# Optimization experiments

Hardware: AMD Instinct MI355X
Metric: run time of the kernel (lower is better)

## Reference

```python
import jax, jax.numpy as jnp
import numpy as np

NUM_HEADS = 16


def setup_inputs() -> dict:
    key = jax.random.key(0)
    k1, k2, k3 = jax.random.split(key, 3)
    B, S, D = 4, 2048, 1024
    x = jax.random.normal(k1, (B, S, D), dtype=jnp.float32)
    w_qkv = jax.random.normal(k2, (D, 3 * D), dtype=jnp.float32) * 0.02
    b_qkv = jnp.zeros((3 * D,), dtype=jnp.float32)
    w_proj = jax.random.normal(k3, (D, D), dtype=jnp.float32) * 0.02
    b_proj = jnp.zeros((D,), dtype=jnp.float32)
    return {"x": x, "w_qkv": w_qkv, "b_qkv": b_qkv, "w_proj": w_proj, "b_proj": b_proj}


def reference(x, w_qkv, b_qkv, w_proj, b_proj):
    B, S, D = x.shape
    H = NUM_HEADS
    hd = D // H
    # fused qkv projection: [B,S,3D] -> [B,S,3H,hd]
    qkv = (x @ w_qkv + b_qkv).reshape(B, S, 3 * H, hd)
    q, k, v = jnp.split(qkv, 3, axis=2)  # each [B,S,H,hd]
    scale = (1.0 / jnp.sqrt(hd)).astype(x.dtype)
    scores = jnp.einsum("bqhd,bkhd->bhqk", q, k) * scale  # [B,H,S,S]
    causal = jnp.tril(jnp.ones((S, S), dtype=bool))  # [S,S]
    masked = jnp.where(causal, scores, jnp.finfo(scores.dtype).min)
    # softmax in fp32 reduce dtype, cast back (dropout_rate=0 -> identity)
    attn = jax.nn.softmax(masked.astype(jnp.float32)).astype(masked.dtype)
    out = jnp.einsum("bhqk,bkhd->bqhd", attn, v).reshape(B, S, D)
    return out @ w_proj + b_proj
```

## Files before the change

### kernel.cpp

```cpp
#include <hip/hip_runtime.h>
#include <hip/hip_bf16.h>

typedef __attribute__((ext_vector_type(8))) short short8;
typedef __attribute__((ext_vector_type(4))) float f32x4;

#define B_   4
#define S_   2048
#define D_   1024
#define H_   16
#define HD_  64
#define M_   (B_ * S_)
#define N3_  (3 * D_)

#define GLDS16(g, l)                                                        \
  __builtin_amdgcn_global_load_lds(                                         \
      (const __attribute__((address_space(1))) void*)(g),                   \
      (__attribute__((address_space(3))) void*)(l), 16, 0, 0)

__device__ __forceinline__ unsigned pack_bf2(float a, float b) {
  union { __hip_bfloat16 h; unsigned short s; } ua, ub;
  ua.h = __float2bfloat16(a);
  ub.h = __float2bfloat16(b);
  return (unsigned)ua.s | ((unsigned)ub.s << 16);
}

__global__ __launch_bounds__(256) void cast_f32_bf16(
    const float* __restrict__ in, __hip_bfloat16* __restrict__ out, int n) {
  int i = (blockIdx.x * 256 + threadIdx.x) * 4;
  if (i + 3 < n) {
    float4 v = *(const float4*)(in + i);
    union { ushort4 u4; __hip_bfloat16 h[4]; } p;
    p.h[0] = __float2bfloat16(v.x);
    p.h[1] = __float2bfloat16(v.y);
    p.h[2] = __float2bfloat16(v.z);
    p.h[3] = __float2bfloat16(v.w);
    *(ushort4*)(out + i) = p.u4;
  }
}

__global__ __launch_bounds__(256) void transpose_cast(
    const float* __restrict__ in, __hip_bfloat16* __restrict__ out,
    int rows, int cols) {
  __shared__ float tile[32][33];
  int bx = blockIdx.x * 32;
  int by = blockIdx.y * 32;
  int tx = threadIdx.x, ty = threadIdx.y;
#pragma unroll
  for (int i = 0; i < 4; ++i)
    tile[ty + i * 8][tx] = in[(size_t)(by + ty + i * 8) * cols + bx + tx];
  __syncthreads();
#pragma unroll
  for (int i = 0; i < 4; ++i)
    out[(size_t)(bx + ty + i * 8) * rows + by + tx] =
        __float2bfloat16(tile[tx][ty + i * 8]);
}

__device__ inline void store_out(float* p, float v) { *p = v; }
__device__ inline void store_out(__hip_bfloat16* p, float v) {
  *p = __float2bfloat16(v);
}

template <typename OUT_T, bool WVT>
__global__ __launch_bounds__(256) void gemm_bt_bias(
    const __hip_bfloat16* __restrict__ A, const __hip_bfloat16* __restrict__ Bt,
    const float* __restrict__ bias, OUT_T* __restrict__ C,
    __hip_bfloat16* __restrict__ vt, int M, int N, int K) {
  __shared__ __align__(16) __hip_bfloat16 Alds[128 * 64];
  __shared__ __align__(16) __hip_bfloat16 Blds[128 * 64];
  const int t = threadIdx.x;
  const int wave = t >> 6, lane = t & 63;
  const int quad = lane >> 4, l15 = lane & 15;
  const int wm = (wave >> 1) * 64, wn = (wave & 1) * 64;
  const int m0 = blockIdx.y * 128, n0 = blockIdx.x * 128;

  const int rsub = lane >> 3;
  const int gc16 = (lane & 7) ^ (rsub & 7);
  const __hip_bfloat16* gA[4];
  const __hip_bfloat16* gB[4];
  __hip_bfloat16* lA[4];
  __hip_bfloat16* lB[4];
#pragma unroll
  for (int i = 0; i < 4; ++i) {
    int c = wave * 4 + i;
    int row = c * 8 + rsub;
    gA[i] = A + (size_t)(m0 + row) * K + gc16 * 8;
    gB[i] = Bt + (size_t)(n0 + row) * K + gc16 * 8;
    lA[i] = Alds + c * 512;
    lB[i] = Blds + c * 512;
  }

  f32x4 acc[4][4] = {};

  for (int k0 = 0; k0 < K; k0 += 64) {
#pragma unroll
    for (int i = 0; i < 4; ++i) {
      GLDS16(gA[i] + k0, lA[i]);
      GLDS16(gB[i] + k0, lB[i]);
    }
    __syncthreads();
#pragma unroll
    for (int kk = 0; kk < 2; ++kk) {
      const int fo = ((kk * 4 + quad) ^ (l15 & 7)) * 8;
      short8 a[4], bfr[4];
#pragma unroll
      for (int mt = 0; mt < 4; ++mt)
        a[mt] = *(const short8*)(Alds + (wm + mt * 16 + l15) * 64 + fo);
#pragma unroll
      for (int nt = 0; nt < 4; ++nt)
        bfr[nt] = *(const short8*)(Blds + (wn + nt * 16 + l15) * 64 + fo);
#pragma unroll
      for (int mt = 0; mt < 4; ++mt)
#pragma unroll
        for (int nt = 0; nt < 4; ++nt)
          acc[mt][nt] = __builtin_amdgcn_mfma_f32_16x16x32_bf16(
              a[mt], bfr[nt], acc[mt][nt], 0, 0, 0);
    }
    __syncthreads();
  }

  if (WVT && n0 >= 2048) {
#pragma unroll
    for (int mt = 0; mt < 4; ++mt)
#pragma unroll
      for (int nt = 0; nt < 4; ++nt) {
        int col = n0 + wn + nt * 16 + l15;
        float bv = bias[col];
        int hv = (col - 2048) >> 6, d = (col - 2048) & 63;
        int row0 = m0 + wm + mt * 16 + quad * 4;
        int bidx = row0 >> 11, s = row0 & 2047;
        uint2 w;
        w.x = pack_bf2(acc[mt][nt][0] + bv, acc[mt][nt][1] + bv);
        w.y = pack_bf2(acc[mt][nt][2] + bv, acc[mt][nt][3] + bv);
        *(uint2*)(vt + ((size_t)(bidx * 16 + hv) * 64 + d) * 2048 + s) = w;
      }
  } else {
#pragma unroll
    for (int mt = 0; mt < 4; ++mt)
#pragma unroll
      for (int nt = 0; nt < 4; ++nt) {
        int col = n0 + wn + nt * 16 + l15;
        float bv = bias[col];
#pragma unroll
        for (int r = 0; r < 4; ++r) {
          int row = m0 + wm + mt * 16 + quad * 4 + r;
          store_out(C + (size_t)row * N + col, acc[mt][nt][r] + bv);
        }
      }
  }
}

__global__ __launch_bounds__(128) void attn_causal(
    const __hip_bfloat16* __restrict__ qkv,
    const __hip_bfloat16* __restrict__ vt,
    __hip_bfloat16* __restrict__ ctx) {
  __shared__ __align__(16) __hip_bfloat16 Klds[64][72];
  __shared__ __align__(16) __hip_bfloat16 Vlds[64][72];
  __shared__ __align__(16) __hip_bfloat16 Plds[2][2][16][72];

  const int t = threadIdx.x;
  const int wave = t >> 6, lane = t & 63;
  const int quad = lane >> 4, l15 = lane & 15;
  const int xb = blockIdx.x, h = blockIdx.y, b = blockIdx.z;

  const size_t qbase = (size_t)b * S_ * N3_ + h * HD_;
  const size_t kbase = qbase + D_;
  const size_t vtbase = (size_t)(b * H_ + h) * HD_ * S_;
  const float C2 = 0.18033688f;

  short8 ones;
#pragma unroll
  for (int j = 0; j < 8; ++j) ones[j] = (short)0x3F80;

  for (int sel = 0; sel < 2; ++sel) {
    const int qb = sel ? (31 - xb) : xb;
    short8 qf[2][2];
#pragma unroll
    for (int g = 0; g < 2; ++g) {
      const int qrow = qb * 64 + wave * 32 + g * 16 + l15;
      qf[g][0] =
          *(const short8*)(qkv + qbase + (size_t)qrow * N3_ + quad * 8);
      qf[g][1] =
          *(const short8*)(qkv + qbase + (size_t)qrow * N3_ + 32 + quad * 8);
    }

    f32x4 o[2][4] = {};
    float m_r[2] = {-1e30f, -1e30f}, l_r[2] = {0.f, 0.f};

    for (int kb = 0; kb <= qb; ++kb) {
#pragma unroll
      for (int i = 0; i < 4; ++i) {
        int c = t + 128 * i;
        int row = c >> 3, seg = c & 7;
        *(uint4*)(&Klds[row][seg * 8]) = *(const uint4*)(
            qkv + kbase + (size_t)(kb * 64 + row) * N3_ + seg * 8);
        *(uint4*)(&Vlds[row][seg * 8]) = *(const uint4*)(
            vt + vtbase + (size_t)row * S_ + kb * 64 + seg * 8);
      }
      __syncthreads();

      short8 kf[4][2];
#pragma unroll
      for (int nt = 0; nt < 4; ++nt) {
        kf[nt][0] = *(const short8*)(&Klds[nt * 16 + l15][quad * 8]);
        kf[nt][1] = *(const short8*)(&Klds[nt * 16 + l15][32 + quad * 8]);
      }

      const bool diag = (kb == qb);
#pragma unroll
      for (int g = 0; g < 2; ++g) {
        f32x4 st[4];
#pragma unroll
        for (int nt = 0; nt < 4; ++nt) {
          f32x4 z = {};
          z = __builtin_amdgcn_mfma_f32_16x16x32_bf16(kf[nt][0], qf[g][0], z,
                                                      0, 0, 0);
          z = __builtin_amdgcn_mfma_f32_16x16x32_bf16(kf[nt][1], qf[g][1], z,
                                                      0, 0, 0);
          st[nt] = z;
        }
        if (diag) {
          const int rloc = wave * 32 + g * 16 + l15;
#pragma unroll
          for (int nt = 0; nt < 4; ++nt)
#pragma unroll
            for (int r = 0; r < 4; ++r)
              if (nt * 16 + quad * 4 + r > rloc) st[nt][r] = -1e30f;
        }

        float tm = st[0][0];
#pragma unroll
        for (int nt = 0; nt < 4; ++nt)
#pragma unroll
          for (int r = 0; r < 4; ++r) tm = fmaxf(tm, st[nt][r]);
        tm = fmaxf(tm, __shfl_xor(tm, 16));
        tm = fmaxf(tm, __shfl_xor(tm, 32));
        const float mn = fmaxf(m_r[g], tm * C2);
        const float alpha = __builtin_amdgcn_exp2f(m_r[g] - mn);
        m_r[g] = mn;
        l_r[g] *= alpha;

#pragma unroll
        for (int nt = 0; nt < 4; ++nt) {
          float p0 = __builtin_amdgcn_exp2f(__builtin_fmaf(st[nt][0], C2, -mn));
          float p1 = __builtin_amdgcn_exp2f(__builtin_fmaf(st[nt][1], C2, -mn));
          float p2 = __builtin_amdgcn_exp2f(__builtin_fmaf(st[nt][2], C2, -mn));
          float p3 = __builtin_amdgcn_exp2f(__builtin_fmaf(st[nt][3], C2, -mn));
          uint2 w;
          w.x = pack_bf2(p0, p1);
          w.y = pack_bf2(p2, p3);
          *(uint2*)(&Plds[wave][g][l15][nt * 16 + quad * 4]) = w;
        }

#pragma unroll
        for (int dt = 0; dt < 4; ++dt)
#pragma unroll
          for (int r = 0; r < 4; ++r) o[g][dt][r] *= alpha;
      }

      short8 pB[2][2];
#pragma unroll
      for (int g = 0; g < 2; ++g) {
        pB[g][0] = *(const short8*)(&Plds[wave][g][l15][quad * 8]);
        pB[g][1] = *(const short8*)(&Plds[wave][g][l15][32 + quad * 8]);
        f32x4 ps = {};
        ps = __builtin_amdgcn_mfma_f32_16x16x32_bf16(ones, pB[g][0], ps, 0, 0, 0);
        ps = __builtin_amdgcn_mfma_f32_16x16x32_bf16(ones, pB[g][1], ps, 0, 0, 0);
        l_r[g] += ps[0];
      }

#pragma unroll
      for (int dt = 0; dt < 4; ++dt) {
        short8 v0 = *(const short8*)(&Vlds[dt * 16 + l15][quad * 8]);
        short8 v1 = *(const short8*)(&Vlds[dt * 16 + l15][32 + quad * 8]);
#pragma unroll
        for (int g = 0; g < 2; ++g) {
          o[g][dt] = __builtin_amdgcn_mfma_f32_16x16x32_bf16(v0, pB[g][0],
                                                             o[g][dt], 0, 0, 0);
          o[g][dt] = __builtin_amdgcn_mfma_f32_16x16x32_bf16(v1, pB[g][1],
                                                             o[g][dt], 0, 0, 0);
        }
      }
      __syncthreads();
    }

#pragma unroll
    for (int g = 0; g < 2; ++g) {
      const float rl = __builtin_amdgcn_rcpf(l_r[g]);
      const int qrow = qb * 64 + wave * 32 + g * 16 + l15;
      __hip_bfloat16* crow = ctx + ((size_t)b * S_ + qrow) * D_ + h * HD_;
#pragma unroll
      for (int dt = 0; dt < 4; ++dt) {
        uint2 w;
        w.x = pack_bf2(o[g][dt][0] * rl, o[g][dt][1] * rl);
        w.y = pack_bf2(o[g][dt][2] * rl, o[g][dt][3] * rl);
        *(uint2*)(crow + dt * 16 + quad * 4) = w;
      }
    }
  }
}

extern "C" void kernel_launch(void* const* d_in, const int* in_sizes, int n_in,
                              void* d_out, int out_size, void* d_ws,
                              size_t ws_size, hipStream_t stream) {
  const float* x      = (const float*)d_in[0];
  const float* w_qkv  = (const float*)d_in[1];
  const float* b_qkv  = (const float*)d_in[2];
  const float* w_proj = (const float*)d_in[3];
  const float* b_proj = (const float*)d_in[4];
  float* out = (float*)d_out;

  char* ws = (char*)d_ws;
  __hip_bfloat16* xb     = (__hip_bfloat16*)(ws + 0);
  __hip_bfloat16* wqkvT  = (__hip_bfloat16*)(ws + 16777216);
  __hip_bfloat16* wprojT = (__hip_bfloat16*)(ws + 23068672);
  __hip_bfloat16* qkvb   = (__hip_bfloat16*)(ws + 25165824);
  __hip_bfloat16* ctx    = (__hip_bfloat16*)(ws + 75497472);
  __hip_bfloat16* vt2    = (__hip_bfloat16*)(ws + 91750400);

  cast_f32_bf16<<<8192, 256, 0, stream>>>(x, xb, M_ * D_);
  transpose_cast<<<dim3(N3_ / 32, D_ / 32), dim3(32, 8), 0, stream>>>(
      w_qkv, wqkvT, D_, N3_);
  transpose_cast<<<dim3(D_ / 32, D_ / 32), dim3(32, 8), 0, stream>>>(
      w_proj, wprojT, D_, D_);

  gemm_bt_bias<__hip_bfloat16, true>
      <<<dim3(N3_ / 128, M_ / 128), 256, 0, stream>>>(
          xb, wqkvT, b_qkv, qkvb, vt2, M_, N3_, D_);

  attn_causal<<<dim3(16, H_, B_), 128, 0, stream>>>(qkvb, vt2, ctx);

  gemm_bt_bias<float, false><<<dim3(D_ / 128, M_ / 128), 256, 0, stream>>>(
      ctx, wprojT, b_proj, out, (__hip_bfloat16*)nullptr, M_, D_, D_);
}
```

Before: 281.7 us.

## Prefetch K/V via global_load_lds with swizzled LDS and lazy softmax rescale

Restructures the causal attention kernel so the next K/V tile streams into LDS through direct global-to-LDS loads while the current tile is computed, with fragments read into registers before the barrier. Removes LDS row padding in favour of an XOR swizzle, and launches one block per query tile (heaviest first) instead of pairing tiles. Also skips the online-softmax rescale unless the running max grows by more than a threshold. The goal is to hide global load latency and cut per-iteration overhead, at the cost of more registers and a lazy-rescale threshold that could affect numerical range.

```diff
diff --git a/kernel.cpp b/kernel.cpp
--- a/kernel.cpp
+++ b/kernel.cpp
@@ -149,18 +149,19 @@
   }
 }
 
-__global__ __launch_bounds__(128) void attn_causal(
+__global__ __launch_bounds__(128, 3) void attn_causal(
     const __hip_bfloat16* __restrict__ qkv,
     const __hip_bfloat16* __restrict__ vt,
     __hip_bfloat16* __restrict__ ctx) {
-  __shared__ __align__(16) __hip_bfloat16 Klds[64][72];
-  __shared__ __align__(16) __hip_bfloat16 Vlds[64][72];
-  __shared__ __align__(16) __hip_bfloat16 Plds[2][2][16][72];
+  __shared__ __align__(16) __hip_bfloat16 Klds[64 * 64];
+  __shared__ __align__(16) __hip_bfloat16 Vlds[64 * 64];
+  __shared__ __align__(16) __hip_bfloat16 Plds[2][2][16][64];
 
   const int t = threadIdx.x;
   const int wave = t >> 6, lane = t & 63;
   const int quad = lane >> 4, l15 = lane & 15;
-  const int xb = blockIdx.x, h = blockIdx.y, b = blockIdx.z;
+  const int qb = 31 - (int)blockIdx.x;
+  const int h = blockIdx.y, b = blockIdx.z;
 
   const size_t qbase = (size_t)b * S_ * N3_ + h * HD_;
   const size_t kbase = qbase + D_;
@@ -171,130 +172,154 @@
 #pragma unroll
   for (int j = 0; j < 8; ++j) ones[j] = (short)0x3F80;
 
-  for (int sel = 0; sel < 2; ++sel) {
-    const int qb = sel ? (31 - xb) : xb;
-    short8 qf[2][2];
+  short8 qf[2][2];
+#pragma unroll
+  for (int g = 0; g < 2; ++g) {
+    const int qrow = qb * 64 + wave * 32 + g * 16 + l15;
+    qf[g][0] = *(const short8*)(qkv + qbase + (size_t)qrow * N3_ + quad * 8);
+    qf[g][1] =
+        *(const short8*)(qkv + qbase + (size_t)qrow * N3_ + 32 + quad * 8);
+  }
+
+  const int rsub = lane >> 3;
+  const int swz = ((lane & 7) ^ rsub) * 8;
+  const __hip_bfloat16* gK[4];
+  const __hip_bfloat16* gV[4];
+  __hip_bfloat16* lK[4];
+  __hip_bfloat16* lV[4];
+#pragma unroll
+  for (int i = 0; i < 4; ++i) {
+    const int c = wave * 4 + i;
+    gK[i] = qkv + kbase + (size_t)(c * 8 + rsub) * N3_ + swz;
+    gV[i] = vt + vtbase + (size_t)(c * 8 + rsub) * S_ + swz;
+    lK[i] = Klds + c * 512;
+    lV[i] = Vlds + c * 512;
+  }
+
+  f32x4 o[2][4] = {};
+  float m_r[2] = {-1e30f, -1e30f}, l_r[2] = {0.f, 0.f};
+
+  const int fo0 = (quad ^ (l15 & 7)) * 8;
+  const int fo1 = ((4 + quad) ^ (l15 & 7)) * 8;
+
+#pragma unroll
+  for (int i = 0; i < 4; ++i) {
+    GLDS16(gK[i], lK[i]);
+    GLDS16(gV[i], lV[i]);
+  }
+  __syncthreads();
+
+  for (int kb = 0; kb <= qb; ++kb) {
+    short8 kf[4][2], vf[4][2];
+#pragma unroll
+    for (int nt = 0; nt < 4; ++nt) {
+      const __hip_bfloat16* kr = Klds + (nt * 16 + l15) * 64;
+      const __hip_bfloat16* vr = Vlds + (nt * 16 + l15) * 64;
+      kf[nt][0] = *(const short8*)(kr + fo0);
+      kf[nt][1] = *(const short8*)(kr + fo1);
+      vf[nt][0] = *(const short8*)(vr + fo0);
+      vf[nt][1] = *(const short8*)(vr + fo1);
+    }
+    __syncthreads();
+    if (kb < qb) {
+#pragma unroll
+      for (int i = 0; i < 4; ++i) {
+        gK[i] += 64 * N3_;
+        gV[i] += 64;
+        GLDS16(gK[i], lK[i]);
+        GLDS16(gV[i], lV[i]);
+      }
+    }
+
+    const bool diag = (kb == qb);
+    short8 pB[2][2];
 #pragma unroll
     for (int g = 0; g < 2; ++g) {
-      const int qrow = qb * 64 + wave * 32 + g * 16 + l15;
-      qf[g][0] =
-          *(const short8*)(qkv + qbase + (size_t)qrow * N3_ + quad * 8);
-      qf[g][1] =
-          *(const short8*)(qkv + qbase + (size_t)qrow * N3_ + 32 + quad * 8);
-    }
-
-    f32x4 o[2][4] = {};
-    float m_r[2] = {-1e30f, -1e30f}, l_r[2] = {0.f, 0.f};
-
-    for (int kb = 0; kb <= qb; ++kb) {
-#pragma unroll
-      for (int i = 0; i < 4; ++i) {
-        int c = t + 128 * i;
-        int row = c >> 3, seg = c & 7;
-        *(uint4*)(&Klds[row][seg * 8]) = *(const uint4*)(
-            qkv + kbase + (size_t)(kb * 64 + row) * N3_ + seg * 8);
-        *(uint4*)(&Vlds[row][seg * 8]) = *(const uint4*)(
-            vt + vtbase + (size_t)row * S_ + kb * 64 + seg * 8);
-      }
-      __syncthreads();
-
-      short8 kf[4][2];
+      f32x4 st[4];
 #pragma unroll
       for (int nt = 0; nt < 4; ++nt) {
-        kf[nt][0] = *(const short8*)(&Klds[nt * 16 + l15][quad * 8]);
-        kf[nt][1] = *(const short8*)(&Klds[nt * 16 + l15][32 + quad * 8]);
-      }
-
-      const bool diag = (kb == qb);
+        f32x4 z = {};
+        z = __builtin_amdgcn_mfma_f32_16x16x32_bf16(kf[nt][0], qf[g][0], z,
+                                                    0, 0, 0);
+        z = __builtin_amdgcn_mfma_f32_16x16x32_bf16(kf[nt][1], qf[g][1], z,
+                                                    0, 0, 0);
+        st[nt] = z;
+      }
+      if (diag) {
+        const int rloc = wave * 32 + g * 16 + l15;
+#pragma unroll
+        for (int nt = 0; nt < 4; ++nt)
+#pragma unroll
+          for (int r = 0; r < 4; ++r)
+            if (nt * 16 + quad * 4 + r > rloc) st[nt][r] = -1e30f;
+      }
+
+      float tm = st[0][0];
+#pragma unroll
+      for (int nt = 0; nt < 4; ++nt)
+#pragma unroll
+        for (int r = 0; r < 4; ++r) tm = fmaxf(tm, st[nt][r]);
+      tm = fmaxf(tm, __shfl_xor(tm, 16));
+      tm = fmaxf(tm, __shfl_xor(tm, 32));
+      const float pm = tm * C2;
+
+      if (!__all(pm - m_r[g] <= 8.0f)) {
+        const float mn = fmaxf(m_r[g], pm);
+        const float al = __builtin_amdgcn_exp2f(m_r[g] - mn);
+        m_r[g] = mn;
+        l_r[g] *= al;
+#pragma unroll
+        for (int dt = 0; dt < 4; ++dt)
+#pragma unroll
+          for (int r = 0; r < 4; ++r) o[g][dt][r] *= al;
+      }
+      const float mneg = -m_r[g];
+
+      __hip_bfloat16* prow = &Plds[wave][g][l15][0];
+#pragma unroll
+      for (int nt = 0; nt < 4; ++nt) {
+        float p0 = __builtin_amdgcn_exp2f(__builtin_fmaf(st[nt][0], C2, mneg));
+        float p1 = __builtin_amdgcn_exp2f(__builtin_fmaf(st[nt][1], C2, mneg));
+        float p2 = __builtin_amdgcn_exp2f(__builtin_fmaf(st[nt][2], C2, mneg));
+        float p3 = __builtin_amdgcn_exp2f(__builtin_fmaf(st[nt][3], C2, mneg));
+        uint2 w;
+        w.x = pack_bf2(p0, p1);
+        w.y = pack_bf2(p2, p3);
+        const int u = nt * 2 + (quad >> 1);
+        *(uint2*)(prow + ((u ^ (l15 & 7)) * 8 + (quad & 1) * 4)) = w;
+      }
+      pB[g][0] = *(const short8*)(prow + fo0);
+      pB[g][1] = *(const short8*)(prow + fo1);
+
+      f32x4 ps = {};
+      ps = __builtin_amdgcn_mfma_f32_16x16x32_bf16(ones, pB[g][0], ps, 0, 0, 0);
+      ps = __builtin_amdgcn_mfma_f32_16x16x32_bf16(ones, pB[g][1], ps, 0, 0, 0);
+      l_r[g] += ps[0];
+    }
+
+#pragma unroll
+    for (int dt = 0; dt < 4; ++dt)
 #pragma unroll
       for (int g = 0; g < 2; ++g) {
-        f32x4 st[4];
-#pragma unroll
-        for (int nt = 0; nt < 4; ++nt) {
-          f32x4 z = {};
-          z = __builtin_amdgcn_mfma_f32_16x16x32_bf16(kf[nt][0], qf[g][0], z,
-                                                      0, 0, 0);
-          z = __builtin_amdgcn_mfma_f32_16x16x32_bf16(kf[nt][1], qf[g][1], z,
-                                                      0, 0, 0);
-          st[nt] = z;
-        }
-        if (diag) {
-          const int rloc = wave * 32 + g * 16 + l15;
-#pragma unroll
-          for (int nt = 0; nt < 4; ++nt)
-#pragma unroll
-            for (int r = 0; r < 4; ++r)
-              if (nt * 16 + quad * 4 + r > rloc) st[nt][r] = -1e30f;
-        }
-
-        float tm = st[0][0];
-#pragma unroll
-        for (int nt = 0; nt < 4; ++nt)
-#pragma unroll
-          for (int r = 0; r < 4; ++r) tm = fmaxf(tm, st[nt][r]);
-        tm = fmaxf(tm, __shfl_xor(tm, 16));
-        tm = fmaxf(tm, __shfl_xor(tm, 32));
-        const float mn = fmaxf(m_r[g], tm * C2);
-        const float alpha = __builtin_amdgcn_exp2f(m_r[g] - mn);
-        m_r[g] = mn;
-        l_r[g] *= alpha;
-
-#pragma unroll
-        for (int nt = 0; nt < 4; ++nt) {
-          float p0 = __builtin_amdgcn_exp2f(__builtin_fmaf(st[nt][0], C2, -mn));
-          float p1 = __builtin_amdgcn_exp2f(__builtin_fmaf(st[nt][1], C2, -mn));
-          float p2 = __builtin_amdgcn_exp2f(__builtin_fmaf(st[nt][2], C2, -mn));
-          float p3 = __builtin_amdgcn_exp2f(__builtin_fmaf(st[nt][3], C2, -mn));
-          uint2 w;
-          w.x = pack_bf2(p0, p1);
-          w.y = pack_bf2(p2, p3);
-          *(uint2*)(&Plds[wave][g][l15][nt * 16 + quad * 4]) = w;
-        }
-
-#pragma unroll
-        for (int dt = 0; dt < 4; ++dt)
-#pragma unroll
-          for (int r = 0; r < 4; ++r) o[g][dt][r] *= alpha;
-      }
-
-      short8 pB[2][2];
-#pragma unroll
-      for (int g = 0; g < 2; ++g) {
-        pB[g][0] = *(const short8*)(&Plds[wave][g][l15][quad * 8]);
-        pB[g][1] = *(const short8*)(&Plds[wave][g][l15][32 + quad * 8]);
-        f32x4 ps = {};
-        ps = __builtin_amdgcn_mfma_f32_16x16x32_bf16(ones, pB[g][0], ps, 0, 0, 0);
-        ps = __builtin_amdgcn_mfma_f32_16x16x32_bf16(ones, pB[g][1], ps, 0, 0, 0);
-        l_r[g] += ps[0];
-      }
-
-#pragma unroll
-      for (int dt = 0; dt < 4; ++dt) {
-        short8 v0 = *(const short8*)(&Vlds[dt * 16 + l15][quad * 8]);
-        short8 v1 = *(const short8*)(&Vlds[dt * 16 + l15][32 + quad * 8]);
-#pragma unroll
-        for (int g = 0; g < 2; ++g) {
-          o[g][dt] = __builtin_amdgcn_mfma_f32_16x16x32_bf16(v0, pB[g][0],
-                                                             o[g][dt], 0, 0, 0);
-          o[g][dt] = __builtin_amdgcn_mfma_f32_16x16x32_bf16(v1, pB[g][1],
-                                                             o[g][dt], 0, 0, 0);
-        }
-      }
-      __syncthreads();
-    }
-
-#pragma unroll
-    for (int g = 0; g < 2; ++g) {
-      const float rl = __builtin_amdgcn_rcpf(l_r[g]);
-      const int qrow = qb * 64 + wave * 32 + g * 16 + l15;
-      __hip_bfloat16* crow = ctx + ((size_t)b * S_ + qrow) * D_ + h * HD_;
-#pragma unroll
-      for (int dt = 0; dt < 4; ++dt) {
-        uint2 w;
-        w.x = pack_bf2(o[g][dt][0] * rl, o[g][dt][1] * rl);
-        w.y = pack_bf2(o[g][dt][2] * rl, o[g][dt][3] * rl);
-        *(uint2*)(crow + dt * 16 + quad * 4) = w;
-      }
+        o[g][dt] = __builtin_amdgcn_mfma_f32_16x16x32_bf16(vf[dt][0], pB[g][0],
+                                                           o[g][dt], 0, 0, 0);
+        o[g][dt] = __builtin_amdgcn_mfma_f32_16x16x32_bf16(vf[dt][1], pB[g][1],
+                                                           o[g][dt], 0, 0, 0);
+      }
+    __syncthreads();
+  }
+
+#pragma unroll
+  for (int g = 0; g < 2; ++g) {
+    const float rl = __builtin_amdgcn_rcpf(l_r[g]);
+    const int qrow = qb * 64 + wave * 32 + g * 16 + l15;
+    __hip_bfloat16* crow = ctx + ((size_t)b * S_ + qrow) * D_ + h * HD_;
+#pragma unroll
+    for (int dt = 0; dt < 4; ++dt) {
+      uint2 w;
+      w.x = pack_bf2(o[g][dt][0] * rl, o[g][dt][1] * rl);
+      w.y = pack_bf2(o[g][dt][2] * rl, o[g][dt][3] * rl);
+      *(uint2*)(crow + dt * 16 + quad * 4) = w;
     }
   }
 }
@@ -327,7 +352,7 @@
       <<<dim3(N3_ / 128, M_ / 128), 256, 0, stream>>>(
           xb, wqkvT, b_qkv, qkvb, vt2, M_, N3_, D_);
 
-  attn_causal<<<dim3(16, H_, B_), 128, 0, stream>>>(qkvb, vt2, ctx);
+  attn_causal<<<dim3(32, H_, B_), 128, 0, stream>>>(qkvb, vt2, ctx);
 
   gemm_bt_bias<float, false><<<dim3(D_ / 128, M_ / 128), 256, 0, stream>>>(
       ctx, wprojT, b_proj, out, (__hip_bfloat16*)nullptr, M_, D_, D_);
```

Result: slower. 309.8 us (+10.0%).
